# Kernel optimization log

Hardware: AMD Instinct MI355X
Metric: run time of the kernel (lower is better)

Reference implementation:

```python
import jax, jax.numpy as jnp
import numpy as np

B = 8192
MOTION_DIM = 512
COMMAND_DIM = 64
HIDDEN = 1024
E = 8  # num_experts
NUM_LAYERS = 6


def _dense(key, shape, fan_in):
    return jax.random.normal(key, shape, dtype=jnp.float32) * (1.0 / np.sqrt(fan_in))


def setup_inputs() -> dict:
    key = jax.random.key(0)
    ks = jax.random.split(key, 32)
    in_dim = MOTION_DIM + COMMAND_DIM  # 576
    inp = {
        "motion": jax.random.normal(ks[0], (B, MOTION_DIM), dtype=jnp.float32),
        "command": jax.random.normal(ks[1], (B, COMMAND_DIM), dtype=jnp.float32),
        # gating network: in -> H -> H -> E, ELU, softmax
        "g_w1": _dense(ks[2], (in_dim, HIDDEN), in_dim),
        "g_b1": jnp.zeros((HIDDEN,), jnp.float32),
        "g_w2": _dense(ks[3], (HIDDEN, HIDDEN), HIDDEN),
        "g_b2": jnp.zeros((HIDDEN,), jnp.float32),
        "g_w3": _dense(ks[4], (HIDDEN, E), HIDDEN),
        "g_b3": jnp.zeros((E,), jnp.float32),
        # MoE layers: dims [in->H, H->H, H->H, H->H, H->H?, ...] per CMG layout
        "w0": _dense(ks[5], (E, in_dim, HIDDEN), in_dim),
        "b0": jnp.zeros((E, HIDDEN), jnp.float32),
        "w1": _dense(ks[6], (E, HIDDEN, HIDDEN), HIDDEN),
        "b1": jnp.zeros((E, HIDDEN), jnp.float32),
        "w2": _dense(ks[7], (E, HIDDEN, HIDDEN), HIDDEN),
        "b2": jnp.zeros((E, HIDDEN), jnp.float32),
        "w3": _dense(ks[8], (E, HIDDEN, HIDDEN), HIDDEN),
        "b3": jnp.zeros((E, HIDDEN), jnp.float32),
        "w4": _dense(ks[9], (E, HIDDEN, HIDDEN), HIDDEN),
        "b4": jnp.zeros((E, HIDDEN), jnp.float32),
        "w5": _dense(ks[10], (E, HIDDEN, MOTION_DIM), HIDDEN),
        "b5": jnp.zeros((E, MOTION_DIM), jnp.float32),
    }
    return inp


def _moe_layer(x, coeffs, W, b):
    # x: [B, din], coeffs: [B, E], W: [E, din, dout], b: [E, dout]
    # y[b] = sum_e coeffs[b,e] * (x[b] @ W[e] + b[e])
    y = jnp.einsum("be,bi,eio->bo", coeffs, x, W)
    y = y + jnp.einsum("be,eo->bo", coeffs, b)
    return y


def _cmg_forward(motion, command,
                 g_w1, g_b1, g_w2, g_b2, g_w3, g_b3,
                 w0, b0, w1, b1, w2, b2, w3, b3, w4, b4, w5, b5):
    x = jnp.concatenate([motion, command], axis=-1)  # [B, in_dim]
    # gating network
    g = jax.nn.elu(x @ g_w1 + g_b1)
    g = jax.nn.elu(g @ g_w2 + g_b2)
    coeffs = jax.nn.softmax(g @ g_w3 + g_b3, axis=-1)  # [B, E]
    # stacked MoE layers with ELU between all but last
    Ws = [w0, w1, w2, w3, w4, w5]
    bs = [b0, b1, b2, b3, b4, b5]
    for i in range(NUM_LAYERS):
        x = _moe_layer(x, coeffs, Ws[i], bs[i])
        if i < NUM_LAYERS - 1:
            x = jax.nn.elu(x)
    return x  # [B, MOTION_DIM]


def reference(motion, command,
              g_w1, g_b1, g_w2, g_b2, g_w3, g_b3,
              w0, b0, w1, b1, w2, b2, w3, b3, w4, b4, w5, b5):
    return _cmg_forward(motion, command,
                        g_w1, g_b1, g_w2, g_b2, g_w3, g_b3,
                        w0, b0, w1, b1, w2, b2, w3, b3, w4, b4, w5, b5)
```

## Files before the change

### kernel.cpp

```cpp
#include <hip/hip_runtime.h>
#include <hip/hip_bf16.h>

typedef __attribute__((ext_vector_type(8))) short bf16x8;
typedef __attribute__((ext_vector_type(4))) float f32x4;

__device__ __forceinline__ float bf2f(unsigned short u) {
    union { unsigned int i; float f; } v; v.i = ((unsigned int)u) << 16; return v.f;
}
__device__ __forceinline__ unsigned short f2bf(float f) {
    union { float f; unsigned int i; } v; v.f = f;
    unsigned int x = v.i;
    return (unsigned short)((x + 0x7FFFu + ((x >> 16) & 1u)) >> 16);
}

__device__ __forceinline__ void gload_lds16(const unsigned short* g, unsigned short* l) {
    __builtin_amdgcn_global_load_lds(
        (const __attribute__((address_space(1))) unsigned int*)g,
        (__attribute__((address_space(3))) unsigned int*)l,
        16, 0, 0);
}

#define VM4  asm volatile("s_waitcnt vmcnt(4)" ::: "memory")
#define VM0  asm volatile("s_waitcnt vmcnt(0)" ::: "memory")
#define LG0  asm volatile("s_waitcnt lgkmcnt(0)" ::: "memory")
#define SB0  __builtin_amdgcn_sched_barrier(0)

__global__ void concat_cvt(const float* __restrict__ motion,
                           const float* __restrict__ command,
                           unsigned short* __restrict__ out) {
    int id = blockIdx.x * 256 + threadIdx.x;
    int b = id / 144, q = id % 144;
    float4 v;
    if (q < 128) v = *(const float4*)(motion + (size_t)b * 512 + q * 4);
    else         v = *(const float4*)(command + (size_t)b * 64 + (q - 128) * 4);
    ushort4 o;
    o.x = f2bf(v.x); o.y = f2bf(v.y); o.z = f2bf(v.z); o.w = f2bf(v.w);
    *(ushort4*)(out + (size_t)b * 576 + q * 4) = o;
}

__global__ void transpose_cvt(const float* __restrict__ in,
                              unsigned short* __restrict__ out,
                              int K, int N, int tpe) {
    __shared__ unsigned short tile[64][72];
    int e = blockIdx.x / tpe, r = blockIdx.x % tpe;
    in  += (size_t)e * K * N;
    out += (size_t)e * N * K;
    int nbn = N / 64;
    int k0 = (r / nbn) * 64;
    int n0 = (r % nbn) * 64;
    int t = threadIdx.x;
    int tx = t & 63, ty = t >> 6;
    #pragma unroll
    for (int rr = 0; rr < 16; ++rr) {
        int kr = ty + rr * 4;
        tile[kr][tx] = f2bf(in[(size_t)(k0 + kr) * N + n0 + tx]);
    }
    __syncthreads();
    int txh = t & 31, tyh = t >> 5;
    #pragma unroll
    for (int rr = 0; rr < 8; ++rr) {
        int nr = tyh + rr * 8;
        unsigned int vlo = tile[2 * txh][nr];
        unsigned int vhi = tile[2 * txh + 1][nr];
        unsigned int* o32 = (unsigned int*)(out + (size_t)(n0 + nr) * K + k0);
        o32[txh] = vlo | (vhi << 16);
    }
}

__global__ __launch_bounds__(256) void gating_kernel(
    const unsigned short* __restrict__ g2,
    const float* __restrict__ w3, const float* __restrict__ b3,
    float* __restrict__ coeffs) {
    __shared__ float w3s[8][1024];
    int t = threadIdx.x;
    for (int i = t; i < 1024; i += 256) {
        #pragma unroll
        for (int e = 0; e < 8; ++e) w3s[e][i] = w3[(size_t)i * 8 + e];
    }
    __syncthreads();
    int lane = t & 63, wv = t >> 6;
    int row = blockIdx.x * 4 + wv;
    const unsigned short* xr = g2 + (size_t)row * 1024;
    float acc[8];
    #pragma unroll
    for (int e = 0; e < 8; ++e) acc[e] = 0.f;
    for (int it = 0; it < 16; ++it) {
        float xv = bf2f(xr[lane + it * 64]);
        #pragma unroll
        for (int e = 0; e < 8; ++e) acc[e] += xv * w3s[e][lane + it * 64];
    }
    #pragma unroll
    for (int e = 0; e < 8; ++e) {
        float v = acc[e];
        #pragma unroll
        for (int off = 32; off; off >>= 1) v += __shfl_xor(v, off);
        acc[e] = v + b3[e];
    }
    float mx = acc[0];
    #pragma unroll
    for (int e = 1; e < 8; ++e) mx = fmaxf(mx, acc[e]);
    float s = 0.f;
    #pragma unroll
    for (int e = 0; e < 8; ++e) { acc[e] = __expf(acc[e] - mx); s += acc[e]; }
    float inv = 1.f / s;
    if (lane < 8) coeffs[(size_t)row * 8 + lane] = acc[lane] * inv;
}

template<bool DO_ELU>
__global__ __launch_bounds__(256, 4)
void gemm_bf16(const unsigned short* __restrict__ A,
               const unsigned short* __restrict__ BT,
               const float* __restrict__ bias,
               unsigned short* __restrict__ Out,
               int N, int ld, int kpart) {
    __shared__ unsigned short As[128 * 64];
    __shared__ unsigned short Bs[128 * 64];
    int ntn = N >> 7;
    int nwg = gridDim.x;
    int bid = blockIdx.x;
    { int cpx = nwg >> 3; bid = (bid & 7) * cpx + (bid >> 3); }
    int tm = bid / ntn, tn = bid - tm * ntn;
    int row0 = tm << 7, col0 = tn << 7;
    int t = threadIdx.x;
    int lane = t & 63;
    int wid = t >> 6;
    int wr = wid >> 1, wc = wid & 1;
    const unsigned short* Ab = A + (size_t)(row0 + wid * 32 + (lane >> 3)) * ld + (lane & 7) * 8;
    const unsigned short* Bb = BT + (size_t)(col0 + wid * 32 + (lane >> 3)) * ld + (lane & 7) * 8;
    unsigned short* Asd = &As[wid * 32 * 64];
    unsigned short* Bsd = &Bs[wid * 32 * 64];
    f32x4 acc[4][4];
    #pragma unroll
    for (int i = 0; i < 4; ++i)
        #pragma unroll
        for (int j = 0; j < 4; ++j) acc[i][j] = (f32x4){0.f, 0.f, 0.f, 0.f};
    int nkt = kpart >> 6;
    for (int kt = 0; kt < nkt; ++kt) {
        size_t ko = (size_t)kt << 6;
        #pragma unroll
        for (int q = 0; q < 4; ++q) {
            gload_lds16(Ab + (size_t)(q * 8) * ld + ko, Asd + q * 8 * 64);
            gload_lds16(Bb + (size_t)(q * 8) * ld + ko, Bsd + q * 8 * 64);
        }
        __syncthreads();
        #pragma unroll
        for (int kk = 0; kk < 2; ++kk) {
            bf16x8 af[4], bfr[4];
            #pragma unroll
            for (int m = 0; m < 4; ++m)
                af[m] = *(const bf16x8*)(&As[(wr * 64 + m * 16 + (lane & 15)) * 64 + kk * 32 + (lane >> 4) * 8]);
            #pragma unroll
            for (int n = 0; n < 4; ++n)
                bfr[n] = *(const bf16x8*)(&Bs[(wc * 64 + n * 16 + (lane & 15)) * 64 + kk * 32 + (lane >> 4) * 8]);
            #pragma unroll
            for (int m = 0; m < 4; ++m)
                #pragma unroll
                for (int n = 0; n < 4; ++n)
                    acc[m][n] = __builtin_amdgcn_mfma_f32_16x16x32_bf16(af[m], bfr[n], acc[m][n], 0, 0, 0);
        }
        __syncthreads();
    }
    #pragma unroll
    for (int m = 0; m < 4; ++m) {
        int rbase = row0 + wr * 64 + m * 16 + ((lane >> 4) << 2);
        #pragma unroll
        for (int n = 0; n < 4; ++n) {
            int cg = col0 + wc * 64 + n * 16 + (lane & 15);
            float bv = bias[cg];
            #pragma unroll
            for (int r2 = 0; r2 < 4; ++r2) {
                float v = acc[m][n][r2] + bv;
                if (DO_ELU) v = v > 0.f ? v : (__expf(v) - 1.f);
                Out[(size_t)(rbase + r2) * N + cg] = f2bf(v);
            }
        }
    }
}

template<bool DO_ELU, bool OUT_F32>
__global__ __launch_bounds__(512, 1)
void gemm_fused(const unsigned short* __restrict__ A,
                const unsigned short* __restrict__ BT,
                const float* __restrict__ coeffs,
                const float* __restrict__ bias,
                void* __restrict__ Out,
                int K, int dout) {
    __shared__ unsigned short lds[65536];

    int ntn = dout >> 5;
    int nwg = gridDim.x;
    int bid = blockIdx.x;
    { int cpx = nwg >> 3; bid = (bid & 7) * cpx + (bid >> 3); }
    int tm = bid / ntn, tn = bid - tm * ntn;
    int row0 = tm << 8;
    int c0 = tn << 5;
    int nkt = K >> 5;

    int t = threadIdx.x;
    int lane = t & 63, wid = t >> 6;
    int wm = wid >> 2, wn = wid & 3;
    int q = lane >> 4;

    int aoff[8], boff[4];
    #pragma unroll
    for (int m = 0; m < 8; ++m) {
        int row = wm * 128 + m * 16 + (lane & 15);
        aoff[m] = row * 32 + ((q ^ ((row >> 1) & 3)) << 3);
    }
    #pragma unroll
    for (int n = 0; n < 4; ++n) {
        int row = wn * 64 + n * 16 + (lane & 15);
        boff[n] = 8192 + row * 32 + ((q ^ ((row >> 1) & 3)) << 3);
    }

    int srow = t >> 2;
    int scol = ((t & 3) ^ ((t >> 3) & 3)) * 8;
    const unsigned short* Asrc = A + (size_t)(row0 + srow) * K + scol;
    int br0 = (srow >> 5) * dout + c0 + (srow & 31);
    int br1 = ((srow + 128) >> 5) * dout + c0 + (srow & 31);
    const unsigned short* Bsrc0 = BT + (size_t)br0 * K + scol;
    const unsigned short* Bsrc1 = BT + (size_t)br1 * K + scol;
    int wdst = wid * 512;

    f32x4 acc[8][4];
    #pragma unroll
    for (int m = 0; m < 8; ++m)
        #pragma unroll
        for (int n = 0; n < 4; ++n) acc[m][n] = (f32x4){0.f, 0.f, 0.f, 0.f};

    #pragma unroll
    for (int S = 0; S < 2; ++S) {
        gload_lds16(Asrc + S * 32,                   &lds[S * 16384 + wdst]);
        gload_lds16(Asrc + (size_t)128 * K + S * 32, &lds[S * 16384 + 4096 + wdst]);
        gload_lds16(Bsrc0 + S * 32,                  &lds[S * 16384 + 8192 + wdst]);
        gload_lds16(Bsrc1 + S * 32,                  &lds[S * 16384 + 12288 + wdst]);
    }
    VM4; SB0;
    __builtin_amdgcn_s_barrier();

    for (int s = 0; s < nkt; ++s) {
        int sb = (s & 3) << 14;
        bool st = (s + 2) < nkt;
        int rb2 = ((s + 2) & 3) << 14;
        int ko2 = (s + 2) * 32;

        bf16x8 bfrg[4], afr[4];
        #pragma unroll
        for (int n = 0; n < 4; ++n)
            bfrg[n] = *(const bf16x8*)(&lds[sb + boff[n]]);
        #pragma unroll
        for (int m = 0; m < 4; ++m)
            afr[m] = *(const bf16x8*)(&lds[sb + aoff[m]]);
        if (st) {
            gload_lds16(Asrc + ko2,                   &lds[rb2 + wdst]);
            gload_lds16(Asrc + (size_t)128 * K + ko2, &lds[rb2 + 4096 + wdst]);
        }
        SB0;
        __builtin_amdgcn_s_barrier();
        LG0; SB0;
        __builtin_amdgcn_s_setprio(1);
        #pragma unroll
        for (int m = 0; m < 4; ++m)
            #pragma unroll
            for (int n = 0; n < 4; ++n)
                acc[m][n] = __builtin_amdgcn_mfma_f32_16x16x32_bf16(bfrg[n], afr[m], acc[m][n], 0, 0, 0);
        __builtin_amdgcn_s_setprio(0);
        __builtin_amdgcn_s_barrier();

        bf16x8 afr2[4];
        #pragma unroll
        for (int m = 0; m < 4; ++m)
            afr2[m] = *(const bf16x8*)(&lds[sb + aoff[m + 4]]);
        if (st) {
            gload_lds16(Bsrc0 + ko2, &lds[rb2 + 8192 + wdst]);
            gload_lds16(Bsrc1 + ko2, &lds[rb2 + 12288 + wdst]);
        }
        SB0;
        if (s + 1 < nkt) {
            if (st) { VM4; } else { VM0; }
        }
        SB0;
        __builtin_amdgcn_s_barrier();
        LG0; SB0;
        __builtin_amdgcn_s_setprio(1);
        #pragma unroll
        for (int m = 0; m < 4; ++m)
            #pragma unroll
            for (int n = 0; n < 4; ++n)
                acc[m + 4][n] = __builtin_amdgcn_mfma_f32_16x16x32_bf16(bfrg[n], afr2[m], acc[m + 4][n], 0, 0, 0);
        __builtin_amdgcn_s_setprio(0);
        __builtin_amdgcn_s_barrier();
    }

    float* plds = (float*)lds;
    __syncthreads();
    {
        int e0 = 2 * wn, e1 = e0 + 1;
        f32x4 b0h[2], b1h[2];
        #pragma unroll
        for (int h = 0; h < 2; ++h) {
            float4 u0 = *(const float4*)(bias + e0 * dout + c0 + h * 16 + q * 4);
            float4 u1 = *(const float4*)(bias + e1 * dout + c0 + h * 16 + q * 4);
            b0h[h] = (f32x4){u0.x, u0.y, u0.z, u0.w};
            b1h[h] = (f32x4){u1.x, u1.y, u1.z, u1.w};
        }
        float* preg = plds + (wid << 12);
        #pragma unroll
        for (int m = 0; m < 8; ++m) {
            int grow = row0 + wm * 128 + m * 16 + (lane & 15);
            float c8 = coeffs[(size_t)grow * 8 + e0];
            float c9 = coeffs[(size_t)grow * 8 + e1];
            #pragma unroll
            for (int h = 0; h < 2; ++h) {
                f32x4 z0 = acc[m][h];
                f32x4 z1 = acc[m][h + 2];
                f32x4 p;
                #pragma unroll
                for (int r = 0; r < 4; ++r)
                    p[r] = c8 * (z0[r] + b0h[h][r]) + c9 * (z1[r] + b1h[h][r]);
                int row = m * 16 + (lane & 15);
                int slot = (h * 4 + q) ^ (row & 7);
                *(f32x4*)(preg + row * 32 + (slot << 2)) = p;
            }
        }
    }
    __syncthreads();

    {
        int r2 = t >> 1;
        int ch = t & 1;
        int wmr = r2 >> 7;
        int rr = r2 & 127;
        int sw = rr & 7;
        size_t obase = (size_t)(row0 + r2) * dout + c0 + ch * 16;
        #pragma unroll
        for (int sl = 0; sl < 4; ++sl) {
            int L = ch * 4 + sl;
            int phys = L ^ sw;
            f32x4 sum = (f32x4){0.f, 0.f, 0.f, 0.f};
            #pragma unroll
            for (int w2 = 0; w2 < 4; ++w2) {
                const f32x4 v = *(const f32x4*)(plds + (((wmr << 2) + w2) << 12) + rr * 32 + (phys << 2));
                sum[0] += v[0]; sum[1] += v[1]; sum[2] += v[2]; sum[3] += v[3];
            }
            if (DO_ELU) {
                #pragma unroll
                for (int r = 0; r < 4; ++r)
                    sum[r] = sum[r] > 0.f ? sum[r] : (__expf(sum[r]) - 1.f);
            }
            if (OUT_F32) {
                float4 o = {sum[0], sum[1], sum[2], sum[3]};
                *(float4*)((float*)Out + obase + sl * 4) = o;
            } else {
                ushort4 o;
                o.x = f2bf(sum[0]); o.y = f2bf(sum[1]);
                o.z = f2bf(sum[2]); o.w = f2bf(sum[3]);
                *(ushort4*)((unsigned short*)Out + obase + sl * 4) = o;
            }
        }
    }
}

extern "C" void kernel_launch(void* const* d_in, const int* in_sizes, int n_in,
                              void* d_out, int out_size, void* d_ws, size_t ws_size,
                              hipStream_t stream) {
    const float* motion  = (const float*)d_in[0];
    const float* command = (const float*)d_in[1];
    const float* g_w1 = (const float*)d_in[2];
    const float* g_b1 = (const float*)d_in[3];
    const float* g_w2 = (const float*)d_in[4];
    const float* g_b2 = (const float*)d_in[5];
    const float* g_w3 = (const float*)d_in[6];
    const float* g_b3 = (const float*)d_in[7];
    const float* w[6]  = {(const float*)d_in[8],  (const float*)d_in[10],
                          (const float*)d_in[12], (const float*)d_in[14],
                          (const float*)d_in[16], (const float*)d_in[18]};
    const float* bb[6] = {(const float*)d_in[9],  (const float*)d_in[11],
                          (const float*)d_in[13], (const float*)d_in[15],
                          (const float*)d_in[17], (const float*)d_in[19]};

    char* ws = (char*)d_ws;
    unsigned short* xc0  = (unsigned short*)ws;
    unsigned short* actA = (unsigned short*)(ws + 9437184);
    unsigned short* actB = (unsigned short*)(ws + 26214400);
    float* coeffs        = (float*)(ws + 42991616);
    unsigned short* wT   = (unsigned short*)(ws + 43253760);

    concat_cvt<<<4608, 256, 0, stream>>>(motion, command, xc0);

    transpose_cvt<<<144, 256, 0, stream>>>(g_w1, wT, 576, 1024, 144);
    gemm_bf16<true><<<512, 256, 0, stream>>>(xc0, wT, g_b1, actA, 1024, 576, 576);
    transpose_cvt<<<256, 256, 0, stream>>>(g_w2, wT, 1024, 1024, 256);
    gemm_bf16<true><<<512, 256, 0, stream>>>(actA, wT, g_b2, actB, 1024, 1024, 1024);
    gating_kernel<<<2048, 256, 0, stream>>>(actB, g_w3, g_b3, coeffs);

    transpose_cvt<<<1152, 256, 0, stream>>>(w[0], wT, 576, 1024, 144);
    gemm_fused<true, false><<<1024, 512, 0, stream>>>(
        xc0, wT, coeffs, bb[0], actA, 576, 1024);

    unsigned short* bufs[2] = {actA, actB};
    for (int l = 1; l <= 4; ++l) {
        unsigned short* in  = bufs[(l + 1) & 1];
        unsigned short* out = bufs[l & 1];
        transpose_cvt<<<2048, 256, 0, stream>>>(w[l], wT, 1024, 1024, 256);
        gemm_fused<true, false><<<1024, 512, 0, stream>>>(
            in, wT, coeffs, bb[l], out, 1024, 1024);
    }

    transpose_cvt<<<1024, 256, 0, stream>>>(w[5], wT, 1024, 512, 128);
    gemm_fused<false, true><<<512, 512, 0, stream>>>(
        actA, wT, coeffs, bb[5], d_out, 1024, 512);
}
```

Measured before the change: 791.5 us.

## Restructure GEMM K-loop into double-buffered 64-wide tiles with split-phase prefetch

The main loop now advances 64 K-elements per iteration instead of 32. The old 4-slot ring with prefetch distance two is replaced by two 64-K buffers, each holding two 32-K sub-tiles. Loads for the next tile are interleaved across four compute phases, B before A, and the prologue now waits for all loads to complete. The aims are lower loop overhead and better overlap of global-to-LDS loads with MFMA work, at the cost of a longer unrolled body and a more delicate vmcnt/barrier ordering.

```diff
diff --git a/kernel.cpp b/kernel.cpp
--- a/kernel.cpp
+++ b/kernel.cpp
@@ -24,6 +24,7 @@
 #define VM0  asm volatile("s_waitcnt vmcnt(0)" ::: "memory")
 #define LG0  asm volatile("s_waitcnt lgkmcnt(0)" ::: "memory")
 #define SB0  __builtin_amdgcn_sched_barrier(0)
+#define BAR  __builtin_amdgcn_s_barrier()
 
 __global__ void concat_cvt(const float* __restrict__ motion,
                            const float* __restrict__ command,
@@ -194,33 +195,33 @@
     int tm = bid / ntn, tn = bid - tm * ntn;
     int row0 = tm << 8;
     int c0 = tn << 5;
-    int nkt = K >> 5;
+    int nkt = K >> 6;
 
     int t = threadIdx.x;
     int lane = t & 63, wid = t >> 6;
     int wm = wid >> 2, wn = wid & 3;
     int q = lane >> 4;
+    int l15 = lane & 15;
 
     int aoff[8], boff[4];
     #pragma unroll
     for (int m = 0; m < 8; ++m) {
-        int row = wm * 128 + m * 16 + (lane & 15);
-        aoff[m] = row * 32 + ((q ^ ((row >> 1) & 3)) << 3);
+        int r = wm * 128 + m * 16 + l15;
+        aoff[m] = r * 32 + ((q ^ ((r >> 1) & 3)) << 3);
     }
     #pragma unroll
     for (int n = 0; n < 4; ++n) {
-        int row = wn * 64 + n * 16 + (lane & 15);
-        boff[n] = 8192 + row * 32 + ((q ^ ((row >> 1) & 3)) << 3);
-    }
-
-    int srow = t >> 2;
-    int scol = ((t & 3) ^ ((t >> 3) & 3)) * 8;
-    const unsigned short* Asrc = A + (size_t)(row0 + srow) * K + scol;
-    int br0 = (srow >> 5) * dout + c0 + (srow & 31);
-    int br1 = ((srow + 128) >> 5) * dout + c0 + (srow & 31);
-    const unsigned short* Bsrc0 = BT + (size_t)br0 * K + scol;
-    const unsigned short* Bsrc1 = BT + (size_t)br1 * K + scol;
-    int wdst = wid * 512;
+        int vr = wn * 64 + n * 16 + l15;
+        boff[n] = 16384 + vr * 32 + ((q ^ ((vr >> 1) & 3)) << 3);
+    }
+
+    int r0 = t >> 2;
+    int sg = ((t & 3) ^ ((t >> 3) & 3)) * 8;
+    const unsigned short* AsrcR0 = A + (size_t)(row0 + r0) * K + sg;
+    const unsigned short* AsrcR1 = AsrcR0 + (size_t)128 * K;
+    int Bh = r0 >> 5, Blow = r0 & 31;
+    const unsigned short* BsrcR0 = BT + ((size_t)(Bh * dout + c0 + Blow)) * K + sg;
+    const unsigned short* BsrcR1 = BT + ((size_t)((Bh + 4) * dout + c0 + Blow)) * K + sg;
 
     f32x4 acc[8][4];
     #pragma unroll
@@ -228,35 +229,38 @@
         #pragma unroll
         for (int n = 0; n < 4; ++n) acc[m][n] = (f32x4){0.f, 0.f, 0.f, 0.f};
 
-    #pragma unroll
-    for (int S = 0; S < 2; ++S) {
-        gload_lds16(Asrc + S * 32,                   &lds[S * 16384 + wdst]);
-        gload_lds16(Asrc + (size_t)128 * K + S * 32, &lds[S * 16384 + 4096 + wdst]);
-        gload_lds16(Bsrc0 + S * 32,                  &lds[S * 16384 + 8192 + wdst]);
-        gload_lds16(Bsrc1 + S * 32,                  &lds[S * 16384 + 12288 + wdst]);
-    }
-    VM4; SB0;
-    __builtin_amdgcn_s_barrier();
-
-    for (int s = 0; s < nkt; ++s) {
-        int sb = (s & 3) << 14;
-        bool st = (s + 2) < nkt;
-        int rb2 = ((s + 2) & 3) << 14;
-        int ko2 = (s + 2) * 32;
+    {
+        gload_lds16(BsrcR0,      &lds[16384 + t * 8]);
+        gload_lds16(BsrcR1,      &lds[16384 + 4096 + t * 8]);
+        gload_lds16(AsrcR0,      &lds[t * 8]);
+        gload_lds16(AsrcR1,      &lds[4096 + t * 8]);
+        gload_lds16(BsrcR0 + 32, &lds[24576 + t * 8]);
+        gload_lds16(BsrcR1 + 32, &lds[24576 + 4096 + t * 8]);
+        gload_lds16(AsrcR0 + 32, &lds[8192 + t * 8]);
+        gload_lds16(AsrcR1 + 32, &lds[8192 + 4096 + t * 8]);
+    }
+    VM0; SB0;
+    BAR;
+
+    for (int T = 0; T < nkt; ++T) {
+        int bb = (T & 1) << 15;
+        int nb = ((T + 1) & 1) << 15;
+        bool st = (T + 1) < nkt;
+        int ko = (T + 1) << 6;
 
         bf16x8 bfrg[4], afr[4];
+
         #pragma unroll
         for (int n = 0; n < 4; ++n)
-            bfrg[n] = *(const bf16x8*)(&lds[sb + boff[n]]);
-        #pragma unroll
-        for (int m = 0; m < 4; ++m)
-            afr[m] = *(const bf16x8*)(&lds[sb + aoff[m]]);
+            bfrg[n] = *(const bf16x8*)(&lds[bb + boff[n]]);
+        #pragma unroll
+        for (int m = 0; m < 4; ++m)
+            afr[m] = *(const bf16x8*)(&lds[bb + aoff[m]]);
         if (st) {
-            gload_lds16(Asrc + ko2,                   &lds[rb2 + wdst]);
-            gload_lds16(Asrc + (size_t)128 * K + ko2, &lds[rb2 + 4096 + wdst]);
-        }
-        SB0;
-        __builtin_amdgcn_s_barrier();
+            gload_lds16(BsrcR0 + ko, &lds[nb + 16384 + t * 8]);
+            gload_lds16(BsrcR1 + ko, &lds[nb + 16384 + 4096 + t * 8]);
+        }
+        SB0; BAR;
         LG0; SB0;
         __builtin_amdgcn_s_setprio(1);
         #pragma unroll
@@ -265,31 +269,68 @@
             for (int n = 0; n < 4; ++n)
                 acc[m][n] = __builtin_amdgcn_mfma_f32_16x16x32_bf16(bfrg[n], afr[m], acc[m][n], 0, 0, 0);
         __builtin_amdgcn_s_setprio(0);
-        __builtin_amdgcn_s_barrier();
-
-        bf16x8 afr2[4];
-        #pragma unroll
-        for (int m = 0; m < 4; ++m)
-            afr2[m] = *(const bf16x8*)(&lds[sb + aoff[m + 4]]);
+        SB0; BAR;
+
+        #pragma unroll
+        for (int m = 0; m < 4; ++m)
+            afr[m] = *(const bf16x8*)(&lds[bb + aoff[m + 4]]);
         if (st) {
-            gload_lds16(Bsrc0 + ko2, &lds[rb2 + 8192 + wdst]);
-            gload_lds16(Bsrc1 + ko2, &lds[rb2 + 12288 + wdst]);
+            gload_lds16(AsrcR0 + ko, &lds[nb + t * 8]);
+            gload_lds16(AsrcR1 + ko, &lds[nb + 4096 + t * 8]);
         }
         SB0;
-        if (s + 1 < nkt) {
-            if (st) { VM4; } else { VM0; }
-        }
-        SB0;
-        __builtin_amdgcn_s_barrier();
+        if (st) { VM4; } else { VM0; }
+        SB0; BAR;
         LG0; SB0;
         __builtin_amdgcn_s_setprio(1);
         #pragma unroll
         for (int m = 0; m < 4; ++m)
             #pragma unroll
             for (int n = 0; n < 4; ++n)
-                acc[m + 4][n] = __builtin_amdgcn_mfma_f32_16x16x32_bf16(bfrg[n], afr2[m], acc[m + 4][n], 0, 0, 0);
+                acc[m + 4][n] = __builtin_amdgcn_mfma_f32_16x16x32_bf16(bfrg[n], afr[m], acc[m + 4][n], 0, 0, 0);
         __builtin_amdgcn_s_setprio(0);
-        __builtin_amdgcn_s_barrier();
+        SB0; BAR;
+
+        #pragma unroll
+        for (int n = 0; n < 4; ++n)
+            bfrg[n] = *(const bf16x8*)(&lds[bb + 8192 + boff[n]]);
+        #pragma unroll
+        for (int m = 0; m < 4; ++m)
+            afr[m] = *(const bf16x8*)(&lds[bb + 8192 + aoff[m]]);
+        if (st) {
+            gload_lds16(BsrcR0 + ko + 32, &lds[nb + 24576 + t * 8]);
+            gload_lds16(BsrcR1 + ko + 32, &lds[nb + 24576 + 4096 + t * 8]);
+        }
+        SB0; BAR;
+        LG0; SB0;
+        __builtin_amdgcn_s_setprio(1);
+        #pragma unroll
+        for (int m = 0; m < 4; ++m)
+            #pragma unroll
+            for (int n = 0; n < 4; ++n)
+                acc[m][n] = __builtin_amdgcn_mfma_f32_16x16x32_bf16(bfrg[n], afr[m], acc[m][n], 0, 0, 0);
+        __builtin_amdgcn_s_setprio(0);
+        SB0; BAR;
+
+        #pragma unroll
+        for (int m = 0; m < 4; ++m)
+            afr[m] = *(const bf16x8*)(&lds[bb + 8192 + aoff[m + 4]]);
+        if (st) {
+            gload_lds16(AsrcR0 + ko + 32, &lds[nb + 8192 + t * 8]);
+            gload_lds16(AsrcR1 + ko + 32, &lds[nb + 8192 + 4096 + t * 8]);
+        }
+        SB0;
+        if (st) { VM4; } else { VM0; }
+        SB0; BAR;
+        LG0; SB0;
+        __builtin_amdgcn_s_setprio(1);
+        #pragma unroll
+        for (int m = 0; m < 4; ++m)
+            #pragma unroll
+            for (int n = 0; n < 4; ++n)
+                acc[m + 4][n] = __builtin_amdgcn_mfma_f32_16x16x32_bf16(bfrg[n], afr[m], acc[m + 4][n], 0, 0, 0);
+        __builtin_amdgcn_s_setprio(0);
+        SB0; BAR;
     }
 
     float* plds = (float*)lds;
@@ -307,7 +348,7 @@
         float* preg = plds + (wid << 12);
         #pragma unroll
         for (int m = 0; m < 8; ++m) {
-            int grow = row0 + wm * 128 + m * 16 + (lane & 15);
+            int grow = row0 + wm * 128 + m * 16 + l15;
             float c8 = coeffs[(size_t)grow * 8 + e0];
             float c9 = coeffs[(size_t)grow * 8 + e1];
             #pragma unroll
@@ -318,7 +359,7 @@
                 #pragma unroll
                 for (int r = 0; r < 4; ++r)
                     p[r] = c8 * (z0[r] + b0h[h][r]) + c9 * (z1[r] + b1h[h][r]);
-                int row = m * 16 + (lane & 15);
+                int row = m * 16 + l15;
                 int slot = (h * 4 + q) ^ (row & 7);
                 *(f32x4*)(preg + row * 32 + (slot << 2)) = p;
             }
```

Result: no change. 793.7 us (+0.3%).
